# Kernel optimization log

Hardware: AMD Instinct MI355X
Metric: run time of the kernel (lower is better)

## Reference

```python
import jax, jax.numpy as jnp
import numpy as np
from jax import lax

# Tree geometry (fixed, mirrors the pickled segment tree):
#   64 leaves x 20 synapses -> 32 intersections -> 32 branches (+8 synapses each)
#   -> 16 -> 8 -> 4 -> 2 intersections -> soma
B, T = 16, 4096
N_LEAF, S_LEAF = 64, 20          # leaf synapses: channels 0..1279
N_BR, S_BR = 32, 8               # branch synapses: channels 1280..1535
C = 8                            # channel_output_number per node
K = 15                           # temporal kernel size
INT_LEVELS = [16, 8, 4, 2]       # intersection fan-in levels above the branch level
NEG_SLOPE = 0.01                 # LeakyReLU default


def _gconv(x, w, b, groups):
    # x: [B, groups*Cin, T], w: [groups*Cout, Cin, K] -> [B, groups*Cout, T]
    y = lax.conv_general_dilated(
        x, w, window_strides=(1,), padding='SAME',
        dimension_numbers=('NCH', 'OIH', 'NCH'),
        feature_group_count=groups)
    return y + b[None, :, None]


def setup_inputs() -> dict:
    key = jax.random.key(0)
    ks = iter(jax.random.split(key, 32))
    sd = 0.05  # init_weights(sd=0.05)
    inp = {'x': jax.random.normal(next(ks), (B, N_LEAF * S_LEAF + N_BR * S_BR, T), jnp.float32)}
    def wb(name, o, i):
        inp['W_' + name] = jax.random.normal(next(ks), (o, i, K), jnp.float32) * sd
        inp['b_' + name] = jax.random.normal(next(ks), (o,), jnp.float32) * sd
    wb('leaf', N_LEAF * C, S_LEAF)            # per-leaf conv: S_LEAF -> C
    wb('int0', N_BR * C, 2 * C)               # 32 intersections merging leaf pairs
    wb('br',   N_BR * C, C + S_BR)            # 32 branch nodes: parent C + S_BR synapses
    for li, n in enumerate(INT_LEVELS):
        wb('int%d' % (li + 1), n * C, 2 * C)
    inp['W_root'] = jax.random.normal(next(ks), (1, 2 * C, 1), jnp.float32) * sd
    inp['b_root'] = jax.random.normal(next(ks), (1,), jnp.float32) * sd
    return inp


def reference(x, W_leaf, b_leaf, W_int0, b_int0, W_br, b_br,
              W_int1, b_int1, W_int2, b_int2, W_int3, b_int3, W_int4, b_int4,
              W_root, b_root):
    act = lambda v: jax.nn.leaky_relu(v, NEG_SLOPE)
    n_leaf_syn = N_LEAF * S_LEAF
    # BRANCH_LEAF level: gather each leaf's synapses (contiguous blocks) -> grouped conv
    h = act(_gconv(x[:, :n_leaf_syn], W_leaf, b_leaf, N_LEAF))          # [B, 64*C, T]
    # BRANCH_INTERSECTION level 0: concat child pairs (adjacent groups) -> grouped conv
    h = act(_gconv(h, W_int0, b_int0, N_BR))                            # [B, 32*C, T]
    # BRANCH level: per-node concat(parent output, gathered synapses) -> grouped conv
    syn = x[:, n_leaf_syn:]                                             # [B, 32*S_BR, T]
    bsz = h.shape[0]
    hb = jnp.concatenate([h.reshape(bsz, N_BR, C, T),
                          syn.reshape(bsz, N_BR, S_BR, T)], axis=2)
    h = act(_gconv(hb.reshape(bsz, N_BR * (C + S_BR), T), W_br, b_br, N_BR))
    # Upper intersection levels: binary merges
    for (W, b), n in zip(((W_int1, b_int1), (W_int2, b_int2), (W_int3, b_int3), (W_int4, b_int4)), INT_LEVELS):
        h = act(_gconv(h, W, b, n))
    # SOMA / RootBlock: concat two children -> 1x1 conv readout
    return _gconv(h, W_root, b_root, 1)                                 # [B, 1, T]
```

## Files before the change

### kernel.cpp

```cpp
#include <hip/hip_runtime.h>
#include <hip/hip_bf16.h>


#define T_LEN 4096
#define KK    15
#define TW    256
#define XS    288
#define SCP   264

typedef __attribute__((ext_vector_type(8))) short    short8;
typedef __attribute__((ext_vector_type(4))) short    short4_t;
typedef __attribute__((ext_vector_type(4))) float    f32x4;
typedef __attribute__((ext_vector_type(2))) unsigned uint2_t;

static __device__ __forceinline__ short f2bf(float f) {
    union { __hip_bfloat16 b; short s; } u; u.b = __float2bfloat16(f); return u.s;
}
static __device__ __forceinline__ float bf2f(short s) {
    union { unsigned u; float f; } u; u.u = ((unsigned)(unsigned short)s) << 16; return u.f;
}

#define MODE_F32   0
#define MODE_BF16  1
#define MODE_SPLIT 2

#define AP_LEAF  0
#define AP_INT0  327680
#define AP_BR    458752
#define AP_INT1  589824
#define AP_INT2  655360
#define AP_INT3  688128
#define AP_INT4  704512
#define AP_TOTAL 712704

__global__ __launch_bounds__(256) void prep_A(
    const float* __restrict__ W0, const float* __restrict__ W1,
    const float* __restrict__ W2, const float* __restrict__ W3,
    const float* __restrict__ W4, const float* __restrict__ W5,
    const float* __restrict__ W6, short* __restrict__ Ap)
{
    const int idx = blockIdx.x * 256 + threadIdx.x;
    if (idx >= AP_TOTAL) return;
    const float* W; int ipg, base;
    if      (idx < AP_INT0) { W = W0; ipg = 20; base = AP_LEAF; }
    else if (idx < AP_BR)   { W = W1; ipg = 16; base = AP_INT0; }
    else if (idx < AP_INT1) { W = W2; ipg = 16; base = AP_BR;   }
    else if (idx < AP_INT2) { W = W3; ipg = 16; base = AP_INT1; }
    else if (idx < AP_INT3) { W = W4; ipg = 16; base = AP_INT2; }
    else if (idx < AP_INT4) { W = W5; ipg = 16; base = AP_INT3; }
    else                    { W = W6; ipg = 16; base = AP_INT4; }
    const int local = idx - base;
    const int e    = local & 7;
    const int fl   = local >> 3;
    const int lane = fl & 63;
    const int fj   = fl >> 6;
    int g, j;
    if (ipg == 20) { g = fj / 10; j = fj - g * 10; }
    else           { g = fj >> 3; j = fj & 7; }
    const int m   = lane & 15;
    const int kap = j * 32 + (lane >> 4) * 8 + e;
    const int ic  = kap >> 4, kp = kap & 15;
    const int k   = kp - (m >> 3);
    float v = 0.f;
    if (k >= 0 && k < KK)
        v = W[((size_t)(g * 8 + (m & 7)) * ipg + ic) * KK + k];
    Ap[idx] = f2bf(v);
}

template <int IPG, int MODE>
__global__ __launch_bounds__(256) void gconv_mfma(
    const void*  __restrict__ inA_, int cinA,
    const float* __restrict__ inX,  int cinX, int xbase,
    const short* __restrict__ Ap,
    const float* __restrict__ bias,
    short* __restrict__ out, int Cout)
{
    constexpr int KD = IPG * 16;
    constexpr int NM = KD / 32;

    __shared__ __align__(16) short s_x[IPG * XS];
    __shared__ __align__(16) short s_a[16 * KD];
    __shared__ __align__(16) short s_c[8 * SCP];

    const int tile = blockIdx.x, g = blockIdx.y, b = blockIdx.z;
    const int tid  = threadIdx.x;
    const int t_base = tile * TW - 8;

    {
        const short* Ag = Ap + (size_t)g * (16 * KD);
        for (int i = tid; i < 2 * KD; i += 256)
            *(short8*)&s_a[i * 8] = *(const short8*)&Ag[i * 8];
    }

    if constexpr (MODE == MODE_BF16) {
        for (int v = tid; v < IPG * 34; v += 256) {
            const int r = v / 34, u = v - r * 34;
            const int gtb = t_base + 8 * u;
            short8 sv = {0, 0, 0, 0, 0, 0, 0, 0};
            if (gtb >= 0 && gtb < T_LEN)
                sv = *(const short8*)((const short*)inA_ +
                      ((size_t)b * cinA + g * IPG + r) * T_LEN + gtb);
            short* row = s_x + r * XS;
            const int p0 = 8 * u;
            if (u > 0) row[p0 - 1] = sv[0];
            uint2_t w;
            w.x = (unsigned short)sv[1] | ((unsigned)(unsigned short)sv[2] << 16);
            w.y = (unsigned short)sv[3] | ((unsigned)(unsigned short)sv[4] << 16);
            *(uint2_t*)(row + p0) = w;
            *(unsigned*)(row + p0 + 4) =
                (unsigned short)sv[5] | ((unsigned)(unsigned short)sv[6] << 16);
            row[p0 + 6] = sv[7];
        }
    } else {
        for (int v = tid; v < IPG * 68; v += 256) {
            const int r = v / 68, u = v - r * 68;
            const int gtb = t_base + 4 * u;
            short h0 = 0, h1 = 0, h2 = 0, h3 = 0;
            if (gtb >= 0 && gtb < T_LEN) {
                if constexpr (MODE == MODE_F32) {
                    f32x4 f = *(const f32x4*)((const float*)inA_ +
                          ((size_t)b * cinA + g * IPG + r) * T_LEN + gtb);
                    h0 = f2bf(f[0]); h1 = f2bf(f[1]); h2 = f2bf(f[2]); h3 = f2bf(f[3]);
                } else {
                    if (r < 8) {
                        short4_t sv = *(const short4_t*)((const short*)inA_ +
                              ((size_t)b * cinA + g * 8 + r) * T_LEN + gtb);
                        h0 = sv[0]; h1 = sv[1]; h2 = sv[2]; h3 = sv[3];
                    } else {
                        f32x4 f = *(const f32x4*)(inX +
                              ((size_t)b * cinX + xbase + g * 8 + (r - 8)) * T_LEN + gtb);
                        h0 = f2bf(f[0]); h1 = f2bf(f[1]); h2 = f2bf(f[2]); h3 = f2bf(f[3]);
                    }
                }
            }
            short* row = s_x + r * XS;
            const int p0 = 4 * u;
            if (u > 0) row[p0 - 1] = h0;
            *(unsigned*)(row + p0) =
                (unsigned short)h1 | ((unsigned)(unsigned short)h2 << 16);
            row[p0 + 2] = h3;
        }
    }
    __syncthreads();

    const int l  = tid & 63;
    const int wv = tid >> 6;
    const int n  = l & 15, q = l >> 4;

    short8 fa[NM];
#pragma unroll
    for (int j = 0; j < NM; ++j)
        fa[j] = *(const short8*)&s_a[(j * 64 + l) * 8];

    float bv[4];
#pragma unroll
    for (int r = 0; r < 4; ++r) bv[r] = bias[g * 8 + ((q * 4 + r) & 7)];

    for (int c = 0; c < 2; ++c) {
        const int co = (wv * 2 + c) * 32;
        f32x4 acc = {bv[0], bv[1], bv[2], bv[3]};
#pragma unroll
        for (int j = 0; j < NM; ++j) {
            const int ic  = j * 2 + (q >> 1);
            const int idx = co + 2 * n + ((q & 1) * 8);
            const unsigned* bp = (const unsigned*)&s_x[ic * XS + idx];
            union { unsigned u[4]; short8 v; } bb;
            bb.u[0] = bp[0]; bb.u[1] = bp[1]; bb.u[2] = bp[2]; bb.u[3] = bp[3];
            acc = __builtin_amdgcn_mfma_f32_16x16x32_bf16(fa[j], bb.v, acc, 0, 0, 0);
        }
#pragma unroll
        for (int r = 0; r < 4; ++r) {
            float vv = acc[r];
            vv = vv > 0.f ? vv : 0.01f * vv;
            const int m = q * 4 + r, oc = m & 7, s = m >> 3;
            s_c[oc * SCP + co + 2 * n + s] = f2bf(vv);
        }
    }
    __syncthreads();

    {
        const int oc = tid >> 5, col = (tid & 31) * 8;
        const short8 vvv = *(const short8*)&s_c[oc * SCP + col];
        *(short8*)(out + ((size_t)b * Cout + g * 8 + oc) * T_LEN + tile * TW + col) = vvv;
    }
}

__global__ __launch_bounds__(256) void root_kernel(
    const short* __restrict__ h,
    const float* __restrict__ W,
    const float* __restrict__ bias,
    float* __restrict__ out)
{
    const int idx = blockIdx.x * 256 + threadIdx.x;
    const int b  = idx >> 10;
    const int t4 = (idx & 1023) * 4;
    const float bb = bias[0];
    float a0 = bb, a1 = bb, a2 = bb, a3 = bb;
#pragma unroll
    for (int ic = 0; ic < 16; ++ic) {
        const short4_t v = *(const short4_t*)&h[((size_t)b * 16 + ic) * T_LEN + t4];
        const float w = W[ic];
        a0 += w * bf2f(v[0]); a1 += w * bf2f(v[1]);
        a2 += w * bf2f(v[2]); a3 += w * bf2f(v[3]);
    }
    f32x4 o = {a0, a1, a2, a3};
    *(f32x4*)&out[(size_t)idx * 4] = o;
}

extern "C" void kernel_launch(void* const* d_in, const int* in_sizes, int n_in,
                              void* d_out, int out_size, void* d_ws, size_t ws_size,
                              hipStream_t stream)
{
    const float* x      = (const float*)d_in[0];
    const float* W_leaf = (const float*)d_in[1];
    const float* b_leaf = (const float*)d_in[2];
    const float* W_int0 = (const float*)d_in[3];
    const float* b_int0 = (const float*)d_in[4];
    const float* W_br   = (const float*)d_in[5];
    const float* b_br   = (const float*)d_in[6];
    const float* W_int1 = (const float*)d_in[7];
    const float* b_int1 = (const float*)d_in[8];
    const float* W_int2 = (const float*)d_in[9];
    const float* b_int2 = (const float*)d_in[10];
    const float* W_int3 = (const float*)d_in[11];
    const float* b_int3 = (const float*)d_in[12];
    const float* W_int4 = (const float*)d_in[13];
    const float* b_int4 = (const float*)d_in[14];
    const float* W_root = (const float*)d_in[15];
    const float* b_root = (const float*)d_in[16];

    short* bufA = (short*)d_ws;
    short* bufB = bufA + (size_t)16 * 512 * 4096;
    short* Ap   = bufB + (size_t)16 * 256 * 4096;

    const int tiles = T_LEN / TW;
    const dim3 blk(256);

    prep_A<<<dim3(AP_TOTAL / 256), blk, 0, stream>>>(
        W_leaf, W_int0, W_br, W_int1, W_int2, W_int3, W_int4, Ap);

    gconv_mfma<20, MODE_F32><<<dim3(tiles, 64, 16), blk, 0, stream>>>(
        x, 1536, nullptr, 0, 0, Ap + AP_LEAF, b_leaf, bufA, 512);
    gconv_mfma<16, MODE_BF16><<<dim3(tiles, 32, 16), blk, 0, stream>>>(
        bufA, 512, nullptr, 0, 0, Ap + AP_INT0, b_int0, bufB, 256);
    gconv_mfma<16, MODE_SPLIT><<<dim3(tiles, 32, 16), blk, 0, stream>>>(
        bufB, 256, x, 1536, 1280, Ap + AP_BR, b_br, bufA, 256);
    gconv_mfma<16, MODE_BF16><<<dim3(tiles, 16, 16), blk, 0, stream>>>(
        bufA, 256, nullptr, 0, 0, Ap + AP_INT1, b_int1, bufB, 128);
    gconv_mfma<16, MODE_BF16><<<dim3(tiles, 8, 16), blk, 0, stream>>>(
        bufB, 128, nullptr, 0, 0, Ap + AP_INT2, b_int2, bufA, 64);
    gconv_mfma<16, MODE_BF16><<<dim3(tiles, 4, 16), blk, 0, stream>>>(
        bufA, 64, nullptr, 0, 0, Ap + AP_INT3, b_int3, bufB, 32);
    gconv_mfma<16, MODE_BF16><<<dim3(tiles, 2, 16), blk, 0, stream>>>(
        bufB, 32, nullptr, 0, 0, Ap + AP_INT4, b_int4, bufA, 16);
    root_kernel<<<dim3((16 * T_LEN / 4) / 256), blk, 0, stream>>>(
        bufA, W_root, b_root, (float*)d_out);
}
```

Before: 661.6 us.

## Load conv B operands directly from global memory, dropping LDS staging

After: 1.653 ms. +149.9%, slower.

```diff
diff --git a/kernel.cpp b/kernel.cpp
--- a/kernel.cpp
+++ b/kernel.cpp
@@ -5,13 +5,12 @@
 #define T_LEN 4096
 #define KK    15
 #define TW    256
-#define XS    288
 #define SCP   264
 
 typedef __attribute__((ext_vector_type(8))) short    short8;
 typedef __attribute__((ext_vector_type(4))) short    short4_t;
 typedef __attribute__((ext_vector_type(4))) float    f32x4;
-typedef __attribute__((ext_vector_type(2))) unsigned uint2_t;
+typedef __attribute__((ext_vector_type(4))) unsigned uint4_t;
 
 static __device__ __forceinline__ short f2bf(float f) {
     union { __hip_bfloat16 b; short s; } u; u.b = __float2bfloat16(f); return u.s;
@@ -67,6 +66,122 @@
     Ap[idx] = f2bf(v);
 }
 
+template <bool INTERIOR>
+static __device__ __forceinline__ short8 load_b_bf16(const short* __restrict__ row, int gt0)
+{
+    unsigned d[5];
+    const int E = gt0 - 1;
+    if constexpr (INTERIOR) {
+        uint4_t dd;
+        __builtin_memcpy(&dd, row + E, 16);
+        d[0] = dd[0]; d[1] = dd[1]; d[2] = dd[2]; d[3] = dd[3];
+        __builtin_memcpy(&d[4], row + E + 8, 4);
+    } else {
+#pragma unroll
+        for (int i = 0; i < 5; ++i) {
+            const int ta = E + 2 * i, tb = ta + 1;
+            const unsigned lo = (ta >= 0 && ta < T_LEN) ? (unsigned short)row[ta] : 0u;
+            const unsigned hi = (tb >= 0 && tb < T_LEN) ? (unsigned short)row[tb] : 0u;
+            d[i] = lo | (hi << 16);
+        }
+    }
+    union { unsigned u[4]; short8 v; } r;
+#pragma unroll
+    for (int i = 0; i < 4; ++i)
+        r.u[i] = __builtin_amdgcn_alignbit(d[i + 1], d[i], 16);
+    return r.v;
+}
+
+template <bool INTERIOR>
+static __device__ __forceinline__ short8 load_b_f32(const float* __restrict__ row, int gt0)
+{
+    float f[8];
+    if constexpr (INTERIOR) {
+        f32x4 a, b;
+        __builtin_memcpy(&a, row + gt0, 16);
+        __builtin_memcpy(&b, row + gt0 + 4, 16);
+        f[0] = a[0]; f[1] = a[1]; f[2] = a[2]; f[3] = a[3];
+        f[4] = b[0]; f[5] = b[1]; f[6] = b[2]; f[7] = b[3];
+    } else {
+#pragma unroll
+        for (int i = 0; i < 8; ++i) {
+            const int t = gt0 + i;
+            f[i] = (t >= 0 && t < T_LEN) ? row[t] : 0.f;
+        }
+    }
+    short8 r;
+#pragma unroll
+    for (int i = 0; i < 8; ++i) r[i] = f2bf(f[i]);
+    return r;
+}
+
+template <int IPG, int MODE, bool INTERIOR>
+static __device__ __forceinline__ void gconv_body(
+    const void* __restrict__ inA_, int cinA,
+    const float* __restrict__ inX, int cinX, int xbase,
+    const short* __restrict__ Ap,
+    const float* __restrict__ bias,
+    short* __restrict__ s_c,
+    int tile, int g, int b, int tid)
+{
+    constexpr int KD = IPG * 16;
+    constexpr int NM = KD / 32;
+
+    const int l  = tid & 63;
+    const int wv = tid >> 6;
+    const int n  = l & 15, q = l >> 4;
+
+    short8 fa[NM];
+    {
+        const short* Ag = Ap + (size_t)g * (16 * KD);
+#pragma unroll
+        for (int j = 0; j < NM; ++j)
+            fa[j] = *(const short8*)&Ag[(j * 64 + l) * 8];
+    }
+
+    float bv[4];
+#pragma unroll
+    for (int r = 0; r < 4; ++r) bv[r] = bias[g * 8 + ((q * 4 + r) & 7)];
+
+    for (int c = 0; c < 2; ++c) {
+        const int co  = (wv * 2 + c) * 32;
+        const int gt0 = tile * TW - 7 + co + 2 * n + 8 * (q & 1);
+        f32x4 acc = {bv[0], bv[1], bv[2], bv[3]};
+#pragma unroll
+        for (int j = 0; j < NM; ++j) {
+            const int ic = j * 2 + (q >> 1);
+            short8 bf;
+            if constexpr (MODE == MODE_F32) {
+                const float* row = (const float*)inA_ +
+                    ((size_t)b * cinA + g * IPG + ic) * T_LEN;
+                bf = load_b_f32<INTERIOR>(row, gt0);
+            } else if constexpr (MODE == MODE_BF16) {
+                const short* row = (const short*)inA_ +
+                    ((size_t)b * cinA + g * IPG + ic) * T_LEN;
+                bf = load_b_bf16<INTERIOR>(row, gt0);
+            } else {
+                if (j < NM / 2) {
+                    const short* row = (const short*)inA_ +
+                        ((size_t)b * cinA + g * 8 + ic) * T_LEN;
+                    bf = load_b_bf16<INTERIOR>(row, gt0);
+                } else {
+                    const float* row = inX +
+                        ((size_t)b * cinX + xbase + g * 8 + (ic - 8)) * T_LEN;
+                    bf = load_b_f32<INTERIOR>(row, gt0);
+                }
+            }
+            acc = __builtin_amdgcn_mfma_f32_16x16x32_bf16(fa[j], bf, acc, 0, 0, 0);
+        }
+#pragma unroll
+        for (int r = 0; r < 4; ++r) {
+            float vv = acc[r];
+            vv = vv > 0.f ? vv : 0.01f * vv;
+            const int m = q * 4 + r, oc = m & 7, s = m >> 3;
+            s_c[oc * SCP + co + 2 * n + s] = f2bf(vv);
+        }
+    }
+}
+
 template <int IPG, int MODE>
 __global__ __launch_bounds__(256) void gconv_mfma(
     const void*  __restrict__ inA_, int cinA,
@@ -75,107 +190,18 @@
     const float* __restrict__ bias,
     short* __restrict__ out, int Cout)
 {
-    constexpr int KD = IPG * 16;
-    constexpr int NM = KD / 32;
-
-    __shared__ __align__(16) short s_x[IPG * XS];
-    __shared__ __align__(16) short s_a[16 * KD];
     __shared__ __align__(16) short s_c[8 * SCP];
 
     const int tile = blockIdx.x, g = blockIdx.y, b = blockIdx.z;
     const int tid  = threadIdx.x;
-    const int t_base = tile * TW - 8;
-
-    {
-        const short* Ag = Ap + (size_t)g * (16 * KD);
-        for (int i = tid; i < 2 * KD; i += 256)
-            *(short8*)&s_a[i * 8] = *(const short8*)&Ag[i * 8];
-    }
-
-    if constexpr (MODE == MODE_BF16) {
-        for (int v = tid; v < IPG * 34; v += 256) {
-            const int r = v / 34, u = v - r * 34;
-            const int gtb = t_base + 8 * u;
-            short8 sv = {0, 0, 0, 0, 0, 0, 0, 0};
-            if (gtb >= 0 && gtb < T_LEN)
-                sv = *(const short8*)((const short*)inA_ +
-                      ((size_t)b * cinA + g * IPG + r) * T_LEN + gtb);
-            short* row = s_x + r * XS;
-            const int p0 = 8 * u;
-            if (u > 0) row[p0 - 1] = sv[0];
-            uint2_t w;
-            w.x = (unsigned short)sv[1] | ((unsigned)(unsigned short)sv[2] << 16);
-            w.y = (unsigned short)sv[3] | ((unsigned)(unsigned short)sv[4] << 16);
-            *(uint2_t*)(row + p0) = w;
-            *(unsigned*)(row + p0 + 4) =
-                (unsigned short)sv[5] | ((unsigned)(unsigned short)sv[6] << 16);
-            row[p0 + 6] = sv[7];
-        }
-    } else {
-        for (int v = tid; v < IPG * 68; v += 256) {
-            const int r = v / 68, u = v - r * 68;
-            const int gtb = t_base + 4 * u;
-            short h0 = 0, h1 = 0, h2 = 0, h3 = 0;
-            if (gtb >= 0 && gtb < T_LEN) {
-                if constexpr (MODE == MODE_F32) {
-                    f32x4 f = *(const f32x4*)((const float*)inA_ +
-                          ((size_t)b * cinA + g * IPG + r) * T_LEN + gtb);
-                    h0 = f2bf(f[0]); h1 = f2bf(f[1]); h2 = f2bf(f[2]); h3 = f2bf(f[3]);
-                } else {
-                    if (r < 8) {
-                        short4_t sv = *(const short4_t*)((const short*)inA_ +
-                              ((size_t)b * cinA + g * 8 + r) * T_LEN + gtb);
-                        h0 = sv[0]; h1 = sv[1]; h2 = sv[2]; h3 = sv[3];
-                    } else {
-                        f32x4 f = *(const f32x4*)(inX +
-                              ((size_t)b * cinX + xbase + g * 8 + (r - 8)) * T_LEN + gtb);
-                        h0 = f2bf(f[0]); h1 = f2bf(f[1]); h2 = f2bf(f[2]); h3 = f2bf(f[3]);
-                    }
-                }
-            }
-            short* row = s_x + r * XS;
-            const int p0 = 4 * u;
-            if (u > 0) row[p0 - 1] = h0;
-            *(unsigned*)(row + p0) =
-                (unsigned short)h1 | ((unsigned)(unsigned short)h2 << 16);
-            row[p0 + 2] = h3;
-        }
-    }
-    __syncthreads();
-
-    const int l  = tid & 63;
-    const int wv = tid >> 6;
-    const int n  = l & 15, q = l >> 4;
-
-    short8 fa[NM];
-#pragma unroll
-    for (int j = 0; j < NM; ++j)
-        fa[j] = *(const short8*)&s_a[(j * 64 + l) * 8];
-
-    float bv[4];
-#pragma unroll
-    for (int r = 0; r < 4; ++r) bv[r] = bias[g * 8 + ((q * 4 + r) & 7)];
-
-    for (int c = 0; c < 2; ++c) {
-        const int co = (wv * 2 + c) * 32;
-        f32x4 acc = {bv[0], bv[1], bv[2], bv[3]};
-#pragma unroll
-        for (int j = 0; j < NM; ++j) {
-            const int ic  = j * 2 + (q >> 1);
-            const int idx = co + 2 * n + ((q & 1) * 8);
-            const unsigned* bp = (const unsigned*)&s_x[ic * XS + idx];
-            union { unsigned u[4]; short8 v; } bb;
-            bb.u[0] = bp[0]; bb.u[1] = bp[1]; bb.u[2] = bp[2]; bb.u[3] = bp[3];
-            acc = __builtin_amdgcn_mfma_f32_16x16x32_bf16(fa[j], bb.v, acc, 0, 0, 0);
-        }
-#pragma unroll
-        for (int r = 0; r < 4; ++r) {
-            float vv = acc[r];
-            vv = vv > 0.f ? vv : 0.01f * vv;
-            const int m = q * 4 + r, oc = m & 7, s = m >> 3;
-            s_c[oc * SCP + co + 2 * n + s] = f2bf(vv);
-        }
-    }
+
+    if (tile > 0 && tile < (int)gridDim.x - 1)
+        gconv_body<IPG, MODE, true >(inA_, cinA, inX, cinX, xbase, Ap, bias,
+                                     s_c, tile, g, b, tid);
+    else
+        gconv_body<IPG, MODE, false>(inA_, cinA, inX, cinX, xbase, Ap, bias,
+                                     s_c, tile, g, b, tid);
+
     __syncthreads();
 
     {
```

## Fuse upper intersection levels and root readout into one LDS-resident kernel

Applied to the files above, without the earlier changes.

After: 650.9 us. Within noise of the previous version (-1.6%).

```diff
diff --git a/kernel.cpp b/kernel.cpp
--- a/kernel.cpp
+++ b/kernel.cpp
@@ -185,26 +185,104 @@
     }
 }
 
-__global__ __launch_bounds__(256) void root_kernel(
-    const short* __restrict__ h,
-    const float* __restrict__ W,
-    const float* __restrict__ bias,
+__device__ __forceinline__ void tail_stage(
+    const short* __restrict__ s_in, int sin_stride,
+    short*       __restrict__ s_out, int sout_stride,
+    const short* __restrict__ ApL, const float* __restrict__ bias,
+    int g, int cbeg, int cend, int tstart, int poff, int t0, int l)
+{
+    const int n = l & 15, q = l >> 4;
+    short8 fa[8];
+    const short* Ag = ApL + (size_t)g * 4096;
+#pragma unroll
+    for (int j = 0; j < 8; ++j)
+        fa[j] = *(const short8*)&Ag[(j * 64 + l) * 8];
+    float bv[4];
+#pragma unroll
+    for (int r = 0; r < 4; ++r) bv[r] = bias[g * 8 + ((q * 4 + r) & 7)];
+
+    for (int c = cbeg; c < cend; ++c) {
+        const int co = c * 32;
+        f32x4 acc = {bv[0], bv[1], bv[2], bv[3]};
+#pragma unroll
+        for (int j = 0; j < 8; ++j) {
+            const int ic = j * 2 + (q >> 1);
+            const unsigned* bp = (const unsigned*)
+                &s_in[(g * 16 + ic) * sin_stride + co + 2 * n + 8 * (q & 1)];
+            union { unsigned u[4]; short8 v; } bb;
+            bb.u[0] = bp[0]; bb.u[1] = bp[1]; bb.u[2] = bp[2]; bb.u[3] = bp[3];
+            acc = __builtin_amdgcn_mfma_f32_16x16x32_bf16(fa[j], bb.v, acc, 0, 0, 0);
+        }
+#pragma unroll
+        for (int r = 0; r < 4; ++r) {
+            const int m = q * 4 + r, oc = m & 7, s = m >> 3;
+            const int t_loc = tstart + co + 2 * n + s;
+            const int gt = t0 + t_loc;
+            float vv = acc[r];
+            vv = vv > 0.f ? vv : 0.01f * vv;
+            const short val = (gt >= 0 && gt < T_LEN) ? f2bf(vv) : (short)0;
+            const int p = t_loc + poff;
+            if (p >= 0)
+                s_out[(g * 8 + oc) * sout_stride + p] = val;
+        }
+    }
+}
+
+__global__ __launch_bounds__(512) void tail_fused(
+    const short* __restrict__ h1,
+    const short* __restrict__ Ap,
+    const float* __restrict__ b2, const float* __restrict__ b3,
+    const float* __restrict__ b4,
+    const float* __restrict__ Wr, const float* __restrict__ br_,
     float* __restrict__ out)
 {
-    const int idx = blockIdx.x * 256 + threadIdx.x;
-    const int b  = idx >> 10;
-    const int t4 = (idx & 1023) * 4;
-    const float bb = bias[0];
-    float a0 = bb, a1 = bb, a2 = bb, a3 = bb;
-#pragma unroll
-    for (int ic = 0; ic < 16; ++ic) {
-        const short4_t v = *(const short4_t*)&h[((size_t)b * 16 + ic) * T_LEN + t4];
-        const float w = W[ic];
-        a0 += w * bf2f(v[0]); a1 += w * bf2f(v[1]);
-        a2 += w * bf2f(v[2]); a3 += w * bf2f(v[3]);
-    }
-    f32x4 o = {a0, a1, a2, a3};
-    *(f32x4*)&out[(size_t)idx * 4] = o;
+    __shared__ __align__(16) short s_mem[65024];
+    short* s_h1 = s_mem;
+    short* s_h3 = s_mem;
+    short* s_h4 = s_mem + 10240;
+    short* s_h2 = s_mem + 44032;
+
+    const int tile = blockIdx.x, b = blockIdx.z;
+    const int tid  = threadIdx.x;
+    const int t0   = tile * 256;
+    const int l = tid & 63, wv = tid >> 6;
+
+    for (int v = tid; v < 128 * 43; v += 512) {
+        const int r = v / 43, u = v - r * 43;
+        const int gt = t0 - 24 + 8 * u;
+        short8 sv = {0, 0, 0, 0, 0, 0, 0, 0};
+        if (gt >= 0 && gt < T_LEN)
+            sv = *(const short8*)&h1[((size_t)b * 128 + r) * T_LEN + gt];
+        short* row = s_h1 + r * 344;
+        const int p0 = 8 * u;
+        if (u > 0) row[p0 - 1] = sv[0];
+        uint2_t w;
+        w.x = (unsigned short)sv[1] | ((unsigned)(unsigned short)sv[2] << 16);
+        w.y = (unsigned short)sv[3] | ((unsigned)(unsigned short)sv[4] << 16);
+        *(uint2_t*)(row + p0) = w;
+        *(unsigned*)(row + p0 + 4) =
+            (unsigned short)sv[5] | ((unsigned)(unsigned short)sv[6] << 16);
+        row[p0 + 6] = sv[7];
+    }
+    __syncthreads();
+
+    tail_stage(s_h1, 344, s_h2, 328, Ap + AP_INT2, b2,
+               wv, 0, 10, -16, 15, t0, l);
+    __syncthreads();
+    tail_stage(s_h2, 328, s_h3, 296, Ap + AP_INT3, b3,
+               wv >> 1, (wv & 1) * 5, (wv & 1) ? 9 : 5, -8, 7, t0, l);
+    __syncthreads();
+    tail_stage(s_h3, 296, s_h4, 264, Ap + AP_INT4, b4,
+               wv >> 2, (wv & 3) * 2, (wv & 3) * 2 + 2, 0, 0, t0, l);
+    __syncthreads();
+
+    if (tid < 256) {
+        float acc = br_[0];
+#pragma unroll
+        for (int ic = 0; ic < 16; ++ic)
+            acc += Wr[ic] * bf2f(s_h4[ic * 264 + tid]);
+        out[(size_t)b * T_LEN + t0 + tid] = acc;
+    }
 }
 
 extern "C" void kernel_launch(void* const* d_in, const int* in_sizes, int n_in,
@@ -247,12 +325,6 @@
         bufB, 256, x, 1536, 1280, Ap + AP_BR, b_br, bufA, 256);
     gconv_mfma<16, MODE_BF16><<<dim3(tiles, 16, 16), blk, 0, stream>>>(
         bufA, 256, nullptr, 0, 0, Ap + AP_INT1, b_int1, bufB, 128);
-    gconv_mfma<16, MODE_BF16><<<dim3(tiles, 8, 16), blk, 0, stream>>>(
-        bufB, 128, nullptr, 0, 0, Ap + AP_INT2, b_int2, bufA, 64);
-    gconv_mfma<16, MODE_BF16><<<dim3(tiles, 4, 16), blk, 0, stream>>>(
-        bufA, 64, nullptr, 0, 0, Ap + AP_INT3, b_int3, bufB, 32);
-    gconv_mfma<16, MODE_BF16><<<dim3(tiles, 2, 16), blk, 0, stream>>>(
-        bufB, 32, nullptr, 0, 0, Ap + AP_INT4, b_int4, bufA, 16);
-    root_kernel<<<dim3((16 * T_LEN / 4) / 256), blk, 0, stream>>>(
-        bufA, W_root, b_root, (float*)d_out);
-}
+    tail_fused<<<dim3(16, 1, 16), dim3(512), 0, stream>>>(
+        bufB, Ap, b_int2, b_int3, b_int4, W_root, b_root, (float*)d_out);
+}
```
